# Optimization experiments

Hardware: AMD Instinct MI355X
Metric: run time of the kernel (lower is better)

The kernel has to match this reference:

```python
import jax, jax.numpy as jnp
import numpy as np

TEMP = 1.75   # temp_schedule(epoch=5, warmup=10): 2.5 - 1.5*0.5
ALPHA = 0.5   # blend_schedule(epoch=5): 0.2 + 0.6*0.5
EPS = 1e-5
HEADS = 2


def _ln(x, g, b):
    mu = x.mean(-1, keepdims=True)
    var = ((x - mu) ** 2).mean(-1, keepdims=True)
    return (x - mu) * jax.lax.rsqrt(var + EPS) * g + b


def _gelu(x):
    return jax.nn.gelu(x, approximate=False)  # torch nn.GELU default = exact erf


def _attn_pool(x, ln_g, ln_b, in_w, in_b, out_w, out_b):
    # x: [N, T, E]; nn.MultiheadAttention self-attention then mean over T
    N, T, E = x.shape
    Dh = E // HEADS
    xn = _ln(x, ln_g, ln_b)
    qkv = xn @ in_w + in_b                      # [N, T, 3E] (in_w stored [E, 3E])
    q, k, v = jnp.split(qkv, 3, axis=-1)
    q = q.reshape(N, T, HEADS, Dh).transpose(0, 2, 1, 3)
    k = k.reshape(N, T, HEADS, Dh).transpose(0, 2, 1, 3)
    v = v.reshape(N, T, HEADS, Dh).transpose(0, 2, 1, 3)
    scores = jnp.einsum('nhqd,nhkd->nhqk', q, k) / jnp.sqrt(jnp.float32(Dh))
    a = jax.nn.softmax(scores, axis=-1)
    o = jnp.einsum('nhqk,nhkd->nhqd', a, v).transpose(0, 2, 1, 3).reshape(N, T, E)
    o = o @ out_w + out_b                       # [N, T, E]
    return o.mean(axis=1)                       # [N, E]


def setup_inputs() -> dict:
    key = jax.random.key(0)
    ks = iter(jax.random.split(key, 40))
    B, L, T, D = 4, 24, 400, 1024
    H = D // 2  # 512
    G = 4       # groups
    s = 0.02
    r = lambda shp: jax.random.normal(next(ks), shp, dtype=jnp.float32) * s
    inp = {
        'x': jax.random.normal(next(ks), (B, L, T, D), dtype=jnp.float32),
        'mlp_alpha': jnp.ones((L,), jnp.float32),
        # shared MLP: LN -> Linear(D,H) -> GELU -> Linear(H,H)
        's_ln_g': jnp.ones((D,), jnp.float32), 's_ln_b': jnp.zeros((D,), jnp.float32),
        's_w1': r((D, H)), 's_b1': jnp.zeros((H,), jnp.float32),
        's_w2': r((H, H)), 's_b2': jnp.zeros((H,), jnp.float32),
        # 4 group MLPs (stacked)
        'g_ln_g': jnp.ones((G, D), jnp.float32), 'g_ln_b': jnp.zeros((G, D), jnp.float32),
        'g_w1': r((G, D, H)), 'g_b1': jnp.zeros((G, H), jnp.float32),
        'g_w2': r((G, H, H)), 'g_b2': jnp.zeros((G, H), jnp.float32),
        # TimeAttentionPool (shared module): LN + MHA(512, 2 heads) + out_proj
        'p_ln_g': jnp.ones((H,), jnp.float32), 'p_ln_b': jnp.zeros((H,), jnp.float32),
        'p_in_w': r((H, 3 * H)), 'p_in_b': jnp.zeros((3 * H,), jnp.float32),
        'p_out_w': r((H, H)), 'p_out_b': jnp.zeros((H,), jnp.float32),
        # router: Linear(512,128) -> GELU -> Linear(128,1) -> sigmoid(/temp)
        'r_w1': r((H, 128)), 'r_b1': jnp.zeros((128,), jnp.float32),
        'r_w2': r((128, 1)), 'r_b2': jnp.zeros((1,), jnp.float32),
        # post norms
        'pn_g': jnp.ones((H,), jnp.float32), 'pn_b': jnp.zeros((H,), jnp.float32),
        'pnf_g': jnp.ones((H,), jnp.float32), 'pnf_b': jnp.zeros((H,), jnp.float32),
        # classifier 512 -> 256 -> 128 -> 2
        'c_w1': r((H, H // 2)), 'c_b1': jnp.zeros((H // 2,), jnp.float32),
        'c_w2': r((H // 2, H // 4)), 'c_b2': jnp.zeros((H // 4,), jnp.float32),
        'c_w3': r((H // 4, 2)), 'c_b3': jnp.zeros((2,), jnp.float32),
    }
    return inp


def reference(x, mlp_alpha, s_ln_g, s_ln_b, s_w1, s_b1, s_w2, s_b2,
              g_ln_g, g_ln_b, g_w1, g_b1, g_w2, g_b2,
              p_ln_g, p_ln_b, p_in_w, p_in_b, p_out_w, p_out_b,
              r_w1, r_b1, r_w2, r_b2, pn_g, pn_b, pnf_g, pnf_b,
              c_w1, c_b1, c_w2, c_b2, c_w3, c_b3):
    B, L, T, D = x.shape
    G = g_w1.shape[0]
    S = L // G  # group_size = 6; expert i uses group i // S
    H = s_w1.shape[1]

    # shared MLP over all experts at once (dropout inactive in eval)
    xs = _ln(x, s_ln_g, s_ln_b)                              # [B,L,T,D]
    shared = _gelu(xs @ s_w1 + s_b1) @ s_w2 + s_b2           # [B,L,T,H]

    # group MLPs: experts i//S -> group; reshape L -> (G, S)
    xg = x.reshape(B, G, S, T, D)
    xgn = _ln(xg, g_ln_g[:, None, None, :], g_ln_b[:, None, None, :])
    hg = _gelu(jnp.einsum('bgstd,gdh->bgsth', xgn, g_w1) + g_b1[None, :, None, None, :])
    grp = jnp.einsum('bgsth,ghk->bgstk', hg, g_w2) + g_b2[None, :, None, None, :]
    grp = grp.reshape(B, L, T, H)

    weighted = shared + mlp_alpha[None, :, None, None] * grp  # [B,L,T,H]

    # attn-pool every expert stream (fold L into batch)
    time_pooled = _attn_pool(weighted.reshape(B * L, T, H),
                             p_ln_g, p_ln_b, p_in_w, p_in_b, p_out_w, p_out_b)
    time_pooled = time_pooled.reshape(B, L, H)               # [B,L,H]

    # router
    rh = _gelu(time_pooled @ r_w1 + r_b1)
    logits_r = (rh @ r_w2 + r_b2)[..., 0]                    # [B,L]
    learned = jax.nn.sigmoid(logits_r / TEMP)
    routing_weights = ALPHA * learned + (1.0 - ALPHA) / L

    # soft fusion over experts
    fusion = (weighted * routing_weights[:, :, None, None]).sum(axis=1)  # [B,T,H]
    fusion = _ln(fusion, pn_g, pn_b).mean(axis=1)            # [B,H]

    shared_mean = shared.mean(axis=1)                        # [B,T,H]
    time_ctx = _attn_pool(shared_mean, p_ln_g, p_ln_b, p_in_w, p_in_b, p_out_w, p_out_b)

    fused_all = _ln(fusion, pnf_g, pnf_b) + _ln(time_ctx, pnf_g, pnf_b)  # [B,H]

    h = _gelu(fused_all @ c_w1 + c_b1)
    h = _gelu(h @ c_w2 + c_b2)
    logits = h @ c_w3 + c_b3                                 # [B,2]
    return logits, routing_weights, fused_all, time_pooled
```

## Files before the change

### kernel.cpp

```cpp
#include <hip/hip_runtime.h>
#include <stdint.h>


typedef float f32x4 __attribute__((ext_vector_type(4)));
typedef short bf16x8 __attribute__((ext_vector_type(8)));

__device__ __forceinline__ float bf2f(unsigned short u) {
  return __uint_as_float(((unsigned int)u) << 16);
}
__device__ __forceinline__ unsigned short f2bf(float f) {
  unsigned int u = __float_as_uint(f);
  u += 0x7fffu + ((u >> 16) & 1u);
  return (unsigned short)(u >> 16);
}
__device__ __forceinline__ float gelu_f(float x) {
  return 0.5f * x * (1.0f + erff(x * 0.70710678118654752440f));
}

typedef __attribute__((address_space(1))) const unsigned int gas_u32;
typedef __attribute__((address_space(3))) unsigned int las_u32;
__device__ __forceinline__ void gload16(const unsigned short* g, unsigned short* l) {
  __builtin_amdgcn_global_load_lds((gas_u32*)g, (las_u32*)l, 16, 0, 0);
}

template <int EPI, int GROUPED>
__global__ __launch_bounds__(256) void gemm_bt(
    const unsigned short* __restrict__ A, const unsigned short* __restrict__ WT,
    const float* __restrict__ bias, unsigned short* __restrict__ Cout,
    const unsigned short* __restrict__ addbuf, const float* __restrict__ alpha_vec,
    unsigned short* __restrict__ vtbuf, int K, int N, int ldout, int Mslice) {
  const int tid = (int)threadIdx.x;
  const int w = tid >> 6, lane = tid & 63, g = lane >> 4, ql = lane & 15;
  const int z = blockIdx.z;
  const int wr = w >> 1, wc = w & 1;

  int bm, bn;
  if (!GROUPED) {
    const int nbm = (int)gridDim.x, nbn = (int)gridDim.y;
    const int nb = nbm * nbn;
    const int lin = (int)blockIdx.x + nbm * (int)blockIdx.y;
    const int q = nb >> 3, r8 = nb & 7;
    const int xcd = lin & 7, c = lin >> 3;
    const int base = (xcd < r8) ? xcd * (q + 1) : r8 * (q + 1) + (xcd - r8) * q;
    const int widx = base + c;
    bm = widx / nbn;
    bn = widx - bm * nbn;
  } else {
    bm = (int)blockIdx.x;
    bn = (int)blockIdx.y;
  }
  const int n0 = bn * 128;

  int rowbase, rows_here;
  const unsigned short* wt = WT;
  const float* bs = bias;
  float alpha = 0.f;
  if (GROUPED) {
    const int l_idx = z % 24;
    const int grp = l_idx / 6;
    rowbase = z * Mslice + bm * 128;
    rows_here = Mslice - bm * 128;
    if (rows_here > 128) rows_here = 128;
    wt = WT + (size_t)grp * (size_t)N * (size_t)K;
    bs = bias + (size_t)grp * (size_t)N;
    if (EPI == 2) alpha = alpha_vec[l_idx];
  } else {
    rowbase = bm * 128;
    rows_here = Mslice - bm * 128;
    if (rows_here > 128) rows_here = 128;
  }

  __shared__ __align__(16) unsigned short sA[2][128 * 32];
  __shared__ __align__(16) unsigned short sB[2][128 * 32];

  f32x4 acc[4][4];
#pragma unroll
  for (int i = 0; i < 4; ++i)
#pragma unroll
    for (int j = 0; j < 4; ++j) acc[i][j] = (f32x4){0.f, 0.f, 0.f, 0.f};

  const int swzg = (lane & 3) ^ ((lane >> 3) & 3);
  const int rA0 = w * 32 + (lane >> 2);
  const int rA1 = rA0 + 16;
  const int rA0c = rA0 < rows_here ? rA0 : rows_here - 1;
  const int rA1c = rA1 < rows_here ? rA1 : rows_here - 1;
  const unsigned short* a0p = A + (size_t)(rowbase + rA0c) * K + swzg * 8;
  const unsigned short* a1p = A + (size_t)(rowbase + rA1c) * K + swzg * 8;
  const unsigned short* b0p = wt + (size_t)(n0 + rA0) * K + swzg * 8;
  const unsigned short* b1p = wt + (size_t)(n0 + rA1) * K + swzg * 8;
  const int ldsw = w * 1024;

  const int aroff = (wr * 64 + ql) * 32 + ((g ^ ((ql >> 1) & 3)) * 8);
  const int broff = (wc * 64 + ql) * 32 + ((g ^ ((ql >> 1) & 3)) * 8);

  const int nsteps = K >> 5;
  gload16(a0p, &sA[0][ldsw]);
  gload16(a1p, &sA[0][ldsw + 512]);
  gload16(b0p, &sB[0][ldsw]);
  gload16(b1p, &sB[0][ldsw + 512]);
  __syncthreads();

  for (int s = 0; s < nsteps; ++s) {
    const int cur = s & 1;
    if (s + 1 < nsteps) {
      const int k0 = (s + 1) << 5;
      const int nxt = cur ^ 1;
      gload16(a0p + k0, &sA[nxt][ldsw]);
      gload16(a1p + k0, &sA[nxt][ldsw + 512]);
      gload16(b0p + k0, &sB[nxt][ldsw]);
      gload16(b1p + k0, &sB[nxt][ldsw + 512]);
    }
    bf16x8 af[4], bfr[4];
#pragma unroll
    for (int mi = 0; mi < 4; ++mi)
      af[mi] = *(const bf16x8*)(&sA[cur][aroff + mi * 512]);
#pragma unroll
    for (int ni = 0; ni < 4; ++ni)
      bfr[ni] = *(const bf16x8*)(&sB[cur][broff + ni * 512]);
#pragma unroll
    for (int mi = 0; mi < 4; ++mi)
#pragma unroll
      for (int ni = 0; ni < 4; ++ni)
        acc[mi][ni] =
            __builtin_amdgcn_mfma_f32_16x16x32_bf16(af[mi], bfr[ni], acc[mi][ni], 0, 0, 0);
    __syncthreads();
  }

#pragma unroll
  for (int mi = 0; mi < 4; ++mi) {
#pragma unroll
    for (int ni = 0; ni < 4; ++ni) {
      const int col = n0 + wc * 64 + ni * 16 + ql;
      const float bb = bs[col];
#pragma unroll
      for (int r = 0; r < 4; ++r) {
        const int rloc = wr * 64 + mi * 16 + 4 * g + r;
        if (rloc >= rows_here) continue;
        const int grow = rowbase + rloc;
        float v = acc[mi][ni][r] + bb;
        if (EPI == 1) v = gelu_f(v);
        if (EPI == 0 || EPI == 1) {
          Cout[(size_t)grow * ldout + col] = f2bf(v);
        } else if (EPI == 2) {
          const float sh = bf2f(addbuf[(size_t)grow * ldout + col]);
          Cout[(size_t)grow * ldout + col] = f2bf(sh + alpha * v);
        } else {
          if (col < 1024) {
            Cout[(size_t)grow * ldout + col] = f2bf(v);
          } else {
            vtbuf[(size_t)grow * 512 + (col - 1024)] = f2bf(v);
          }
        }
      }
    }
  }
}

__global__ void transpose_v(const unsigned short* __restrict__ vbuf,
                            unsigned short* __restrict__ vt) {
  const int p = blockIdx.z;
  const int h = p & 1, nst = p >> 1;
  const int t0 = blockIdx.x * 32, d0 = blockIdx.y * 32;
  __shared__ unsigned short tile[32][33];
  const int tx = threadIdx.x, ty = threadIdx.y;
#pragma unroll
  for (int i = 0; i < 4; ++i) {
    const int t = t0 + ty + i * 8;
    if (t < 400)
      tile[ty + i * 8][tx] = vbuf[((size_t)nst * 400 + t) * 512 + h * 256 + d0 + tx];
  }
  __syncthreads();
  const int t = t0 + tx;
  if (t < 400) {
#pragma unroll
    for (int i = 0; i < 4; ++i)
      vt[((size_t)p * 256 + d0 + ty + i * 8) * 400 + t] = tile[tx][ty + i * 8];
  }
}

__global__ __launch_bounds__(256, 2) void attn_fwd(const unsigned short* __restrict__ qk,
                                                   const unsigned short* __restrict__ vt,
                                                   unsigned short* __restrict__ outb) {
  const int nb = (int)gridDim.x;
  int flat = (int)blockIdx.x;
  flat = (flat & 7) * (nb >> 3) + (flat >> 3);
  const int qt = flat % 7;
  const int h = (flat / 7) & 1;
  const int n = flat / 14;
  const int q0 = qt * 64;

  const int tid = (int)threadIdx.x;
  const int w = tid >> 6, lane = tid & 63, g = lane >> 4, ql = lane & 15;

  __shared__ __align__(16) unsigned short slab[400 * 32];
  __shared__ __align__(16) unsigned short Pc[4][512];
  __shared__ float rs[4][16];

  const int qr = q0 + w * 16 + ql;
  const int qrc = qr < 400 ? qr : 399;
  const unsigned short* qp = qk + ((size_t)n * 400 + qrc) * 1024 + h * 256 + g * 8;
  bf16x8 qf[8];
#pragma unroll
  for (int d0 = 0; d0 < 8; ++d0) qf[d0] = *(const bf16x8*)(qp + d0 * 32);

  f32x4 st[25];
#pragma unroll
  for (int kf = 0; kf < 25; ++kf) st[kf] = (f32x4){0.f, 0.f, 0.f, 0.f};

  const unsigned short* kbase = qk + (size_t)n * 400 * 1024 + 512 + h * 256;
  for (int d0 = 0; d0 < 8; ++d0) {
    bf16x8 stg[7];
#pragma unroll
    for (int c = 0; c < 7; ++c) {
      const int q = tid + c * 256;
      const int r = q >> 2, slot = q & 3;
      if (r < 400)
        stg[c] = *(const bf16x8*)(kbase + (size_t)r * 1024 + d0 * 32 + slot * 8);
    }
    __syncthreads();
#pragma unroll
    for (int c = 0; c < 7; ++c) {
      const int q = tid + c * 256;
      const int r = q >> 2, slot = q & 3;
      if (r < 400) *(bf16x8*)(slab + r * 32 + (slot ^ ((r >> 1) & 3)) * 8) = stg[c];
    }
    __syncthreads();
#pragma unroll
    for (int kf = 0; kf < 25; ++kf) {
      const int r = kf * 16 + ql;
      bf16x8 kfr = *(const bf16x8*)(slab + r * 32 + ((g ^ ((r >> 1) & 3)) * 8));
      st[kf] = __builtin_amdgcn_mfma_f32_16x16x32_bf16(kfr, qf[d0], st[kf], 0, 0, 0);
    }
  }

  const float sc = 0.0625f;
  float m = -3.0e38f;
#pragma unroll
  for (int kf = 0; kf < 25; ++kf)
    m = fmaxf(m, fmaxf(fmaxf(st[kf][0], st[kf][1]), fmaxf(st[kf][2], st[kf][3])));
  m = fmaxf(m, __shfl_xor(m, 16));
  m = fmaxf(m, __shfl_xor(m, 32));
  float sum = 0.f;
  uint2 pp[25];
#pragma unroll
  for (int kf = 0; kf < 25; ++kf) {
    float e0 = expf((st[kf][0] - m) * sc);
    float e1 = expf((st[kf][1] - m) * sc);
    float e2 = expf((st[kf][2] - m) * sc);
    float e3 = expf((st[kf][3] - m) * sc);
    sum += (e0 + e1) + (e2 + e3);
    pp[kf].x = (unsigned int)f2bf(e0) | ((unsigned int)f2bf(e1) << 16);
    pp[kf].y = (unsigned int)f2bf(e2) | ((unsigned int)f2bf(e3) << 16);
  }
  sum += __shfl_xor(sum, 16);
  sum += __shfl_xor(sum, 32);
  if (g == 0) rs[w][ql] = sum;

  f32x4 oacc[16];
#pragma unroll
  for (int nf = 0; nf < 16; ++nf) oacc[nf] = (f32x4){0.f, 0.f, 0.f, 0.f};

  unsigned short* Pw = Pc[w];
  const unsigned short* vbase = vt + (size_t)(n * 2 + h) * 256 * 400;
  for (int kt = 0; kt < 13; ++kt) {
    const int k0 = kt * 32;
    bf16x8 stg[4];
#pragma unroll
    for (int c = 0; c < 4; ++c) {
      const int q = tid + c * 256;
      const int r = q >> 2, slot = q & 3;
      int kc = k0 + slot * 8;
      if (kc >= 400) kc = 0;
      stg[c] = *(const bf16x8*)(vbase + (size_t)r * 400 + kc);
    }
    __syncthreads();
#pragma unroll
    for (int c = 0; c < 4; ++c) {
      const int q = tid + c * 256;
      const int r = q >> 2, slot = q & 3;
      *(bf16x8*)(slab + r * 32 + (slot ^ ((r >> 1) & 3)) * 8) = stg[c];
    }
    {
      const int kf0 = 2 * kt;
      *(uint2*)(Pw + ql * 32 + 4 * g) = pp[kf0];
      uint2 hi = (kf0 + 1 < 25) ? pp[kf0 + 1] : (uint2){0u, 0u};
      *(uint2*)(Pw + ql * 32 + 16 + 4 * g) = hi;
    }
    __syncthreads();
    bf16x8 pa = *(const bf16x8*)(Pw + ql * 32 + g * 8);
#pragma unroll
    for (int nf = 0; nf < 16; ++nf) {
      const int r = nf * 16 + ql;
      bf16x8 vb = *(const bf16x8*)(slab + r * 32 + ((g ^ ((r >> 1) & 3)) * 8));
      oacc[nf] = __builtin_amdgcn_mfma_f32_16x16x32_bf16(pa, vb, oacc[nf], 0, 0, 0);
    }
  }

  const float inv0 = 1.f / rs[w][4 * g + 0];
  const float inv1 = 1.f / rs[w][4 * g + 1];
  const float inv2 = 1.f / rs[w][4 * g + 2];
  const float inv3 = 1.f / rs[w][4 * g + 3];
#pragma unroll
  for (int nf = 0; nf < 16; ++nf) {
#pragma unroll
    for (int r = 0; r < 4; ++r) {
      const int qrow = q0 + w * 16 + 4 * g + r;
      if (qrow < 400) {
        const float invr = (r == 0) ? inv0 : (r == 1) ? inv1 : (r == 2) ? inv2 : inv3;
        outb[((size_t)n * 400 + qrow) * 512 + h * 256 + nf * 16 + ql] =
            f2bf(oacc[nf][r] * invr);
      }
    }
  }
}

template <int TIN, int TOUT>
__global__ void ln_rows(const void* __restrict__ inv, void* __restrict__ outv,
                        const float* __restrict__ gam, const float* __restrict__ bet,
                        int C) {
  const int row = blockIdx.x, t = (int)threadIdx.x;
  float x0, x1, x2, x3;
  if (TIN == 0) {
    float4 v = ((const float4*)inv)[(size_t)row * (C >> 2) + t];
    x0 = v.x; x1 = v.y; x2 = v.z; x3 = v.w;
  } else {
    ushort4 v = ((const ushort4*)inv)[(size_t)row * (C >> 2) + t];
    x0 = bf2f(v.x); x1 = bf2f(v.y); x2 = bf2f(v.z); x3 = bf2f(v.w);
  }
  float s1 = x0 + x1 + x2 + x3;
  float s2 = x0 * x0 + x1 * x1 + x2 * x2 + x3 * x3;
  for (int mlane = 1; mlane < 64; mlane <<= 1) {
    s1 += __shfl_xor(s1, mlane);
    s2 += __shfl_xor(s2, mlane);
  }
  __shared__ float red[8];
  const int nw = blockDim.x >> 6;
  if ((t & 63) == 0) {
    red[t >> 6] = s1;
    red[4 + (t >> 6)] = s2;
  }
  __syncthreads();
  s1 = 0.f; s2 = 0.f;
  for (int i = 0; i < nw; ++i) {
    s1 += red[i];
    s2 += red[4 + i];
  }
  const float mu = s1 / C;
  const float var = s2 / C - mu * mu;
  const float rstd = rsqrtf(var + 1e-5f);
  float y0 = (x0 - mu) * rstd, y1 = (x1 - mu) * rstd, y2 = (x2 - mu) * rstd,
        y3 = (x3 - mu) * rstd;
  if (gam) {
    const int c = t * 4;
    y0 = y0 * gam[c + 0] + bet[c + 0];
    y1 = y1 * gam[c + 1] + bet[c + 1];
    y2 = y2 * gam[c + 2] + bet[c + 2];
    y3 = y3 * gam[c + 3] + bet[c + 3];
  }
  if (TOUT == 0) {
    ushort4 o;
    o.x = f2bf(y0); o.y = f2bf(y1); o.z = f2bf(y2); o.w = f2bf(y3);
    ((ushort4*)outv)[(size_t)row * (C >> 2) + t] = o;
  } else {
    float4 o;
    o.x = y0; o.y = y1; o.z = y2; o.w = y3;
    ((float4*)outv)[(size_t)row * (C >> 2) + t] = o;
  }
}

__global__ void transpose_w(const float* __restrict__ W, const float* __restrict__ scale,
                            unsigned short* __restrict__ WT, int K, int N) {
  __shared__ float tile[32][33];
  const int k0 = blockIdx.x * 32, n0 = blockIdx.y * 32, zg = blockIdx.z;
  const float* Wz = W + (size_t)zg * K * N;
  const float* sz = scale ? scale + (size_t)zg * K : (const float*)0;
  unsigned short* WTz = WT + (size_t)zg * (size_t)K * N;
  const int tx = threadIdx.x, ty = threadIdx.y;
#pragma unroll
  for (int i = 0; i < 4; ++i)
    tile[ty + i * 8][tx] = Wz[(size_t)(k0 + ty + i * 8) * N + n0 + tx];
  __syncthreads();
#pragma unroll
  for (int i = 0; i < 4; ++i) {
    const int nn = n0 + ty + i * 8;
    const int kk = k0 + tx;
    float v = tile[tx][ty + i * 8];
    if (sz) v *= sz[kk];
    WTz[(size_t)nn * K + kk] = f2bf(v);
  }
}

__global__ void transpose_wf(const float* __restrict__ W, float* __restrict__ WT, int K,
                             int N) {
  __shared__ float tile[32][33];
  const int k0 = blockIdx.x * 32, n0 = blockIdx.y * 32;
  const int tx = threadIdx.x, ty = threadIdx.y;
#pragma unroll
  for (int i = 0; i < 4; ++i) {
    const int k = k0 + ty + i * 8;
    if (k < K && n0 + tx < N) tile[ty + i * 8][tx] = W[(size_t)k * N + n0 + tx];
  }
  __syncthreads();
#pragma unroll
  for (int i = 0; i < 4; ++i) {
    const int nn = n0 + ty + i * 8;
    const int kk = k0 + tx;
    if (nn < N && kk < K) WT[(size_t)nn * K + kk] = tile[tx][ty + i * 8];
  }
}

#define BF_KC 16
__global__ void bias_fold_part(const float* __restrict__ W, const float* __restrict__ lb,
                               float* __restrict__ part, int K, int N) {
  const int zg = blockIdx.z;
  const int n = blockIdx.x * 256 + (int)threadIdx.x;
  const int kc = blockIdx.y;
  const int kpc = K / BF_KC;
  const float* Wz = W + (size_t)zg * K * N;
  const float* lbz = lb + (size_t)zg * K;
  float acc = 0.f;
  const int k1 = (kc + 1) * kpc;
  for (int k = kc * kpc; k < k1; ++k) acc += lbz[k] * Wz[(size_t)k * N + n];
  part[((size_t)zg * BF_KC + kc) * N + n] = acc;
}
__global__ void bias_fold_final(const float* __restrict__ part, const float* __restrict__ b,
                                float* __restrict__ beff, int N) {
  const int zg = blockIdx.y;
  const int n = blockIdx.x * 256 + (int)threadIdx.x;
  float acc = b[(size_t)zg * N + n];
#pragma unroll
  for (int c = 0; c < BF_KC; ++c) acc += part[((size_t)zg * BF_KC + c) * N + n];
  beff[(size_t)zg * N + n] = acc;
}

__global__ void mean_l(const unsigned short* __restrict__ sh, float* __restrict__ out) {
  const int i = blockIdx.x * 256 + (int)threadIdx.x;
  if (i >= 4 * 400 * 512 / 4) return;
  const int b = i / (400 * 512 / 4);
  const int rem4 = i - b * (400 * 512 / 4);
  float a0 = 0.f, a1 = 0.f, a2 = 0.f, a3 = 0.f;
  for (int l = 0; l < 24; ++l) {
    ushort4 v = *(const ushort4*)(sh + (size_t)(b * 24 + l) * 204800 + rem4 * 4);
    a0 += bf2f(v.x); a1 += bf2f(v.y); a2 += bf2f(v.z); a3 += bf2f(v.w);
  }
  float4 o;
  o.x = a0 * (1.f / 24.f); o.y = a1 * (1.f / 24.f);
  o.z = a2 * (1.f / 24.f); o.w = a3 * (1.f / 24.f);
  ((float4*)out)[i] = o;
}

__global__ void mean_t_bf16(const unsigned short* __restrict__ in, float* __restrict__ out,
                            int Ns) {
  const int i = blockIdx.x * 256 + (int)threadIdx.x;
  if (i >= Ns * 512) return;
  const int nstr = i >> 9, c = i & 511;
  float acc = 0.f;
  for (int t = 0; t < 400; ++t) acc += bf2f(in[((size_t)nstr * 400 + t) * 512 + c]);
  out[i] = acc * (1.f / 400.f);
}

__global__ void mean_t_f32(const float* __restrict__ in, float* __restrict__ out, int Ns) {
  const int i = blockIdx.x * 256 + (int)threadIdx.x;
  if (i >= Ns * 512) return;
  const int nstr = i >> 9, c = i & 511;
  float acc = 0.f;
  for (int t = 0; t < 400; ++t) acc += in[((size_t)nstr * 400 + t) * 512 + c];
  out[i] = acc * (1.f / 400.f);
}

__global__ void fuse_k(const unsigned short* __restrict__ wgt, const float* __restrict__ rw,
                       float* __restrict__ out) {
  const int i = blockIdx.x * 256 + (int)threadIdx.x;
  if (i >= 4 * 400 * 512 / 4) return;
  const int b = i / (400 * 512 / 4);
  const int rem4 = i - b * (400 * 512 / 4);
  float a0 = 0.f, a1 = 0.f, a2 = 0.f, a3 = 0.f;
  for (int l = 0; l < 24; ++l) {
    const float wv = rw[b * 24 + l];
    ushort4 v = *(const ushort4*)(wgt + (size_t)(b * 24 + l) * 204800 + rem4 * 4);
    a0 += wv * bf2f(v.x); a1 += wv * bf2f(v.y);
    a2 += wv * bf2f(v.z); a3 += wv * bf2f(v.w);
  }
  float4 o;
  o.x = a0; o.y = a1; o.z = a2; o.w = a3;
  ((float4*)out)[i] = o;
}

template <int WLAYOUT>
__global__ void gemv_wave(const float* __restrict__ A, const float* __restrict__ Wm,
                          const float* __restrict__ b, float* __restrict__ C, int M, int K,
                          int N, int act) {
  const int wid = (int)(blockIdx.x * (blockDim.x >> 6)) + ((int)threadIdx.x >> 6);
  const int lane = (int)threadIdx.x & 63;
  if (wid >= M * N) return;
  const int row = wid / N, col = wid - row * N;
  const float* a = A + (size_t)row * K;
  float acc = 0.f;
  if (WLAYOUT) {
    const float* wt = Wm + (size_t)col * K;
    for (int k = lane; k < K; k += 64) acc += a[k] * wt[k];
  } else {
    for (int k = lane; k < K; k += 64) acc += a[k] * Wm[(size_t)k * N + col];
  }
#pragma unroll
  for (int d = 1; d < 64; d <<= 1) acc += __shfl_xor(acc, d);
  if (lane == 0) {
    acc += b[col];
    if (act) acc = gelu_f(acc);
    C[wid] = acc;
  }
}

__global__ void routing_k(const float* __restrict__ lr, float* __restrict__ o1,
                          float* __restrict__ o2) {
  const int i = (int)threadIdx.x;
  if (i < 96) {
    const float v = 0.5f / (1.f + expf(-lr[i] * (1.f / 1.75f))) + (0.5f / 24.f);
    o1[i] = v;
    o2[i] = v;
  }
}

__global__ void add_k(const float* __restrict__ a, const float* __restrict__ b,
                      float* __restrict__ o1, float* __restrict__ o2, int n) {
  const int i = blockIdx.x * 256 + (int)threadIdx.x;
  if (i < n) {
    const float v = a[i] + b[i];
    o1[i] = v;
    o2[i] = v;
  }
}

extern "C" void kernel_launch(void* const* d_in, const int* in_sizes, int n_in,
                              void* d_out, int out_size, void* d_ws, size_t ws_size,
                              hipStream_t stream) {
  const float* x = (const float*)d_in[0];
  const float* mlp_alpha = (const float*)d_in[1];
  const float* s_ln_g = (const float*)d_in[2];
  const float* s_ln_b = (const float*)d_in[3];
  const float* s_w1 = (const float*)d_in[4];
  const float* s_b1 = (const float*)d_in[5];
  const float* s_w2 = (const float*)d_in[6];
  const float* s_b2 = (const float*)d_in[7];
  const float* g_ln_g = (const float*)d_in[8];
  const float* g_ln_b = (const float*)d_in[9];
  const float* g_w1 = (const float*)d_in[10];
  const float* g_b1 = (const float*)d_in[11];
  const float* g_w2 = (const float*)d_in[12];
  const float* g_b2 = (const float*)d_in[13];
  const float* p_ln_g = (const float*)d_in[14];
  const float* p_ln_b = (const float*)d_in[15];
  const float* p_in_w = (const float*)d_in[16];
  const float* p_in_b = (const float*)d_in[17];
  const float* p_out_w = (const float*)d_in[18];
  const float* p_out_b = (const float*)d_in[19];
  const float* r_w1 = (const float*)d_in[20];
  const float* r_b1 = (const float*)d_in[21];
  const float* r_w2 = (const float*)d_in[22];
  const float* r_b2 = (const float*)d_in[23];
  const float* pn_g = (const float*)d_in[24];
  const float* pn_b = (const float*)d_in[25];
  const float* pnf_g = (const float*)d_in[26];
  const float* pnf_b = (const float*)d_in[27];
  const float* c_w1 = (const float*)d_in[28];
  const float* c_b1 = (const float*)d_in[29];
  const float* c_w2 = (const float*)d_in[30];
  const float* c_b2 = (const float*)d_in[31];
  const float* c_w3 = (const float*)d_in[32];
  const float* c_b3 = (const float*)d_in[33];

  float* out = (float*)d_out;
  uint8_t* ws = (uint8_t*)d_ws;

  size_t off = 0;
  auto alloc = [&](size_t bytes) -> size_t {
    size_t o = off;
    off += (bytes + 255) & ~(size_t)255;
    return o;
  };
  const size_t off_xhat = alloc(38400ull * 1024 * 2);
  const size_t off_h = alloc(38400ull * 512 * 2);
  const size_t off_shared = alloc(38400ull * 512 * 2);
  const size_t off_weighted = alloc(38400ull * 512 * 2);
  const size_t off_qk = alloc(38400ull * 1024 * 2);
  const size_t off_pooled = alloc(96ull * 512 * 4);
  const size_t off_rh = alloc(96ull * 128 * 4);
  const size_t off_lr = alloc(96ull * 4);
  const size_t off_rw = alloc(96ull * 4);
  const size_t off_smean = alloc(4ull * 400 * 512 * 4);
  const size_t off_wn2 = alloc(1600ull * 512 * 2);
  const size_t off_qk2 = alloc(1600ull * 1024 * 2);
  const size_t off_vbuf2 = alloc(1600ull * 512 * 2);
  const size_t off_vt2 = alloc(4ull * 2 * 256 * 400 * 2);
  const size_t off_ao2 = alloc(1600ull * 512 * 2);
  const size_t off_pooled2 = alloc(4ull * 512 * 4);
  const size_t off_tctx = alloc(4ull * 512 * 4);
  const size_t off_fusion = alloc(4ull * 400 * 512 * 4);
  const size_t off_fln = alloc(4ull * 400 * 512 * 4);
  const size_t off_fvec = alloc(4ull * 512 * 4);
  const size_t off_fa = alloc(4ull * 512 * 4);
  const size_t off_fb = alloc(4ull * 512 * 4);
  const size_t off_fall = alloc(4ull * 512 * 4);
  const size_t off_c1 = alloc(4ull * 256 * 4);
  const size_t off_c2 = alloc(4ull * 128 * 4);
  const size_t off_sw1T = alloc(512ull * 1024 * 2);
  const size_t off_sw2T = alloc(512ull * 512 * 2);
  const size_t off_gw1T = alloc(4ull * 512 * 1024 * 2);
  const size_t off_gw2T = alloc(4ull * 512 * 512 * 2);
  const size_t off_pinT = alloc(1536ull * 512 * 2);
  const size_t off_sb1e = alloc(512ull * 4);
  const size_t off_gb1e = alloc(4ull * 512 * 4);
  const size_t off_pinbe = alloc(1536ull * 4);
  const size_t off_bfp_s = alloc((size_t)BF_KC * 512 * 4);
  const size_t off_bfp_g = alloc(4ull * BF_KC * 512 * 4);
  const size_t off_bfp_p = alloc((size_t)BF_KC * 1536 * 4);
  const size_t off_powT = alloc(512ull * 512 * 4);
  const size_t off_rw1T = alloc(128ull * 512 * 4);
  const size_t off_cw1T = alloc(256ull * 512 * 4);
  const size_t off_cw2T = alloc(128ull * 256 * 4);
  const size_t off_wn = off_xhat;
  const size_t off_vbuf = off_xhat + 38400ull * 512 * 2;
  const size_t off_vt = off_shared;
  const size_t off_ao = off_h;
  if (off > ws_size) return;

  unsigned short* xhat = (unsigned short*)(ws + off_xhat);
  unsigned short* hbuf = (unsigned short*)(ws + off_h);
  unsigned short* sharedb = (unsigned short*)(ws + off_shared);
  unsigned short* weighted = (unsigned short*)(ws + off_weighted);
  unsigned short* qk = (unsigned short*)(ws + off_qk);
  unsigned short* wn = (unsigned short*)(ws + off_wn);
  unsigned short* vbuf = (unsigned short*)(ws + off_vbuf);
  unsigned short* vt = (unsigned short*)(ws + off_vt);
  unsigned short* ao = (unsigned short*)(ws + off_ao);
  float* pooled = (float*)(ws + off_pooled);
  float* rh = (float*)(ws + off_rh);
  float* lr = (float*)(ws + off_lr);
  float* rw = (float*)(ws + off_rw);
  float* smean = (float*)(ws + off_smean);
  unsigned short* wn2 = (unsigned short*)(ws + off_wn2);
  unsigned short* qk2 = (unsigned short*)(ws + off_qk2);
  unsigned short* vbuf2 = (unsigned short*)(ws + off_vbuf2);
  unsigned short* vt2 = (unsigned short*)(ws + off_vt2);
  unsigned short* ao2 = (unsigned short*)(ws + off_ao2);
  float* pooled2 = (float*)(ws + off_pooled2);
  float* tctx = (float*)(ws + off_tctx);
  float* fusion = (float*)(ws + off_fusion);
  float* fln = (float*)(ws + off_fln);
  float* fvec = (float*)(ws + off_fvec);
  float* fa = (float*)(ws + off_fa);
  float* fb = (float*)(ws + off_fb);
  float* fall = (float*)(ws + off_fall);
  float* c1 = (float*)(ws + off_c1);
  float* c2 = (float*)(ws + off_c2);
  unsigned short* sw1T = (unsigned short*)(ws + off_sw1T);
  unsigned short* sw2T = (unsigned short*)(ws + off_sw2T);
  unsigned short* gw1T = (unsigned short*)(ws + off_gw1T);
  unsigned short* gw2T = (unsigned short*)(ws + off_gw2T);
  unsigned short* pinT = (unsigned short*)(ws + off_pinT);
  float* sb1e = (float*)(ws + off_sb1e);
  float* gb1e = (float*)(ws + off_gb1e);
  float* pinbe = (float*)(ws + off_pinbe);
  float* bfp_s = (float*)(ws + off_bfp_s);
  float* bfp_g = (float*)(ws + off_bfp_g);
  float* bfp_p = (float*)(ws + off_bfp_p);
  float* powT = (float*)(ws + off_powT);
  float* rw1T = (float*)(ws + off_rw1T);
  float* cw1T = (float*)(ws + off_cw1T);
  float* cw2T = (float*)(ws + off_cw2T);

  transpose_w<<<dim3(32, 16, 1), dim3(32, 8), 0, stream>>>(s_w1, s_ln_g, sw1T, 1024, 512);
  transpose_w<<<dim3(16, 16, 1), dim3(32, 8), 0, stream>>>(s_w2, (const float*)0, sw2T, 512, 512);
  transpose_w<<<dim3(32, 16, 4), dim3(32, 8), 0, stream>>>(g_w1, g_ln_g, gw1T, 1024, 512);
  transpose_w<<<dim3(16, 16, 4), dim3(32, 8), 0, stream>>>(g_w2, (const float*)0, gw2T, 512, 512);
  transpose_w<<<dim3(16, 48, 1), dim3(32, 8), 0, stream>>>(p_in_w, p_ln_g, pinT, 512, 1536);
  transpose_wf<<<dim3(16, 16), dim3(32, 8), 0, stream>>>(p_out_w, powT, 512, 512);
  transpose_wf<<<dim3(16, 4), dim3(32, 8), 0, stream>>>(r_w1, rw1T, 512, 128);
  transpose_wf<<<dim3(16, 8), dim3(32, 8), 0, stream>>>(c_w1, cw1T, 512, 256);
  transpose_wf<<<dim3(8, 4), dim3(32, 8), 0, stream>>>(c_w2, cw2T, 256, 128);
  bias_fold_part<<<dim3(2, BF_KC, 1), 256, 0, stream>>>(s_w1, s_ln_b, bfp_s, 1024, 512);
  bias_fold_final<<<dim3(2, 1), 256, 0, stream>>>(bfp_s, s_b1, sb1e, 512);
  bias_fold_part<<<dim3(2, BF_KC, 4), 256, 0, stream>>>(g_w1, g_ln_b, bfp_g, 1024, 512);
  bias_fold_final<<<dim3(2, 4), 256, 0, stream>>>(bfp_g, g_b1, gb1e, 512);
  bias_fold_part<<<dim3(6, BF_KC, 1), 256, 0, stream>>>(p_in_w, p_ln_b, bfp_p, 512, 1536);
  bias_fold_final<<<dim3(6, 1), 256, 0, stream>>>(bfp_p, p_in_b, pinbe, 1536);

  ln_rows<0, 0><<<38400, 256, 0, stream>>>(x, xhat, (const float*)0, (const float*)0, 1024);

  gemm_bt<1, 0><<<dim3(300, 4, 1), 256, 0, stream>>>(xhat, sw1T, sb1e, hbuf,
      (const unsigned short*)0, (const float*)0, (unsigned short*)0, 1024, 512, 512, 38400);
  gemm_bt<0, 0><<<dim3(300, 4, 1), 256, 0, stream>>>(hbuf, sw2T, s_b2, sharedb,
      (const unsigned short*)0, (const float*)0, (unsigned short*)0, 512, 512, 512, 38400);
  mean_l<<<800, 256, 0, stream>>>(sharedb, smean);

  gemm_bt<1, 1><<<dim3(4, 4, 96), 256, 0, stream>>>(xhat, gw1T, gb1e, hbuf,
      (const unsigned short*)0, (const float*)0, (unsigned short*)0, 1024, 512, 512, 400);
  gemm_bt<2, 1><<<dim3(4, 4, 96), 256, 0, stream>>>(hbuf, gw2T, g_b2, weighted,
      sharedb, mlp_alpha, (unsigned short*)0, 512, 512, 512, 400);

  ln_rows<1, 0><<<38400, 128, 0, stream>>>(weighted, wn, (const float*)0, (const float*)0, 512);
  gemm_bt<3, 0><<<dim3(300, 12, 1), 256, 0, stream>>>(wn, pinT, pinbe, qk,
      (const unsigned short*)0, (const float*)0, vbuf, 512, 1536, 1024, 38400);
  transpose_v<<<dim3(13, 8, 192), dim3(32, 8), 0, stream>>>(vbuf, vt);
  attn_fwd<<<dim3(14 * 96), 256, 0, stream>>>(qk, vt, ao);
  mean_t_bf16<<<192, 256, 0, stream>>>(ao, pooled, 96);
  gemv_wave<1><<<12288, 256, 0, stream>>>(pooled, powT, p_out_b, out + 2152, 96, 512, 512, 0);

  gemv_wave<1><<<3072, 256, 0, stream>>>(out + 2152, rw1T, r_b1, rh, 96, 512, 128, 1);
  gemv_wave<0><<<24, 256, 0, stream>>>(rh, r_w2, r_b2, lr, 96, 128, 1, 0);
  routing_k<<<1, 128, 0, stream>>>(lr, out + 8, rw);

  fuse_k<<<800, 256, 0, stream>>>(weighted, rw, fusion);
  ln_rows<0, 1><<<1600, 128, 0, stream>>>(fusion, fln, pn_g, pn_b, 512);
  mean_t_f32<<<8, 256, 0, stream>>>(fln, fvec, 4);

  ln_rows<0, 0><<<1600, 128, 0, stream>>>(smean, wn2, (const float*)0, (const float*)0, 512);
  gemm_bt<3, 0><<<dim3(13, 12, 1), 256, 0, stream>>>(wn2, pinT, pinbe, qk2,
      (const unsigned short*)0, (const float*)0, vbuf2, 512, 1536, 1024, 1600);
  transpose_v<<<dim3(13, 8, 8), dim3(32, 8), 0, stream>>>(vbuf2, vt2);
  attn_fwd<<<dim3(14 * 4), 256, 0, stream>>>(qk2, vt2, ao2);
  mean_t_bf16<<<8, 256, 0, stream>>>(ao2, pooled2, 4);
  gemv_wave<1><<<512, 256, 0, stream>>>(pooled2, powT, p_out_b, tctx, 4, 512, 512, 0);

  ln_rows<0, 1><<<4, 128, 0, stream>>>(fvec, fa, pnf_g, pnf_b, 512);
  ln_rows<0, 1><<<4, 128, 0, stream>>>(tctx, fb, pnf_g, pnf_b, 512);
  add_k<<<8, 256, 0, stream>>>(fa, fb, out + 104, fall, 2048);

  gemv_wave<1><<<256, 256, 0, stream>>>(fall, cw1T, c_b1, c1, 4, 512, 256, 1);
  gemv_wave<1><<<128, 256, 0, stream>>>(c1, cw2T, c_b2, c2, 4, 256, 128, 1);
  gemv_wave<0><<<2, 256, 0, stream>>>(c2, c_w3, c_b3, out, 4, 128, 2, 0);
}
```

Baseline: 821.1 us.

## Triple-buffer GEMM LDS tiles with prefetch distance two and vmcnt waits

Switches the bf16 MFMA GEMM from double to triple buffering in LDS, so loads run two k-steps ahead. It uses explicit s_waitcnt vmcnt counters and raw s_barrier instead of __syncthreads, which lets outstanding global-to-LDS loads overlap more compute. The cost is 50% more LDS per block, which may lower occupancy. The hand-written waitcnt/barrier ordering also has to stay correct across the loop (two barriers per step).

```diff
diff --git a/kernel.cpp b/kernel.cpp
--- a/kernel.cpp
+++ b/kernel.cpp
@@ -70,8 +70,8 @@
     if (rows_here > 128) rows_here = 128;
   }
 
-  __shared__ __align__(16) unsigned short sA[2][128 * 32];
-  __shared__ __align__(16) unsigned short sB[2][128 * 32];
+  __shared__ __align__(16) unsigned short sA[3][128 * 32];
+  __shared__ __align__(16) unsigned short sB[3][128 * 32];
 
   f32x4 acc[4][4];
 #pragma unroll
@@ -98,32 +98,42 @@
   gload16(a1p, &sA[0][ldsw + 512]);
   gload16(b0p, &sB[0][ldsw]);
   gload16(b1p, &sB[0][ldsw + 512]);
-  __syncthreads();
+  gload16(a0p + 32, &sA[1][ldsw]);
+  gload16(a1p + 32, &sA[1][ldsw + 512]);
+  gload16(b0p + 32, &sB[1][ldsw]);
+  gload16(b1p + 32, &sB[1][ldsw + 512]);
 
   for (int s = 0; s < nsteps; ++s) {
-    const int cur = s & 1;
     if (s + 1 < nsteps) {
-      const int k0 = (s + 1) << 5;
-      const int nxt = cur ^ 1;
-      gload16(a0p + k0, &sA[nxt][ldsw]);
-      gload16(a1p + k0, &sA[nxt][ldsw + 512]);
-      gload16(b0p + k0, &sB[nxt][ldsw]);
-      gload16(b1p + k0, &sB[nxt][ldsw + 512]);
+      asm volatile("s_waitcnt vmcnt(4)" ::: "memory");
+    } else {
+      asm volatile("s_waitcnt vmcnt(0)" ::: "memory");
+    }
+    __builtin_amdgcn_s_barrier();
+    const int cb = s % 3;
+    if (s + 2 < nsteps) {
+      const int pb = (s + 2) % 3;
+      const int k0 = (s + 2) << 5;
+      gload16(a0p + k0, &sA[pb][ldsw]);
+      gload16(a1p + k0, &sA[pb][ldsw + 512]);
+      gload16(b0p + k0, &sB[pb][ldsw]);
+      gload16(b1p + k0, &sB[pb][ldsw + 512]);
     }
     bf16x8 af[4], bfr[4];
 #pragma unroll
     for (int mi = 0; mi < 4; ++mi)
-      af[mi] = *(const bf16x8*)(&sA[cur][aroff + mi * 512]);
+      af[mi] = *(const bf16x8*)(&sA[cb][aroff + mi * 512]);
 #pragma unroll
     for (int ni = 0; ni < 4; ++ni)
-      bfr[ni] = *(const bf16x8*)(&sB[cur][broff + ni * 512]);
+      bfr[ni] = *(const bf16x8*)(&sB[cb][broff + ni * 512]);
 #pragma unroll
     for (int mi = 0; mi < 4; ++mi)
 #pragma unroll
       for (int ni = 0; ni < 4; ++ni)
         acc[mi][ni] =
             __builtin_amdgcn_mfma_f32_16x16x32_bf16(af[mi], bfr[ni], acc[mi][ni], 0, 0, 0);
-    __syncthreads();
+    __builtin_amdgcn_sched_barrier(0);
+    __builtin_amdgcn_s_barrier();
   }
 
 #pragma unroll
```

Measured after the change: 853.3 us. 1.04x slower.
